# Kernel optimization log

Hardware: AMD Instinct MI355X
Metric: run time of the kernel (lower is better)

Reference implementation:

```python
import jax, jax.numpy as jnp
import numpy as np

DIM, HEADS, DIM_HEAD = 1024, 16, 64


def setup_inputs() -> dict:
    key = jax.random.key(0)
    k1, k2, k3, k4 = jax.random.split(key, 4)
    x = jax.random.normal(k1, (4, 2048, DIM), dtype=jnp.float32)
    # nn.Linear(dim, 3*dim, bias=False): weight [3*dim, dim]; y = x @ W.T
    W_qkv = jax.random.normal(k2, (3 * DIM, DIM), dtype=jnp.float32) * (DIM ** -0.5)
    W_proj = jax.random.normal(k3, (DIM, DIM), dtype=jnp.float32) * (DIM ** -0.5)
    b_proj = jax.random.normal(k4, (DIM,), dtype=jnp.float32) * 0.02
    return {"x": x, "W_qkv": W_qkv, "W_proj": W_proj, "b_proj": b_proj}


def reference(x, W_qkv, W_proj, b_proj):
    B, N, C = x.shape
    H, D = HEADS, DIM_HEAD
    scale = D ** -0.5
    qkv = x @ W_qkv.T                                   # [B, N, 3C]
    qkv = qkv.reshape(B, N, 3, H, D).transpose(2, 0, 3, 1, 4)  # [3, B, H, N, D]
    q, k, v = qkv[0], qkv[1], qkv[2]
    dots = jnp.einsum('bhid,bhjd->bhij', q, k) * scale  # [B, H, N, N]
    attn = jax.nn.softmax(dots, axis=-1)
    out = jnp.einsum('bhij,bhjd->bhid', attn, v)        # [B, H, N, D]
    out = out.transpose(0, 2, 1, 3).reshape(B, N, C)
    return out @ W_proj.T + b_proj
```

## Files before the change

kernel.cpp:

```cpp
#include <hip/hip_runtime.h>
#include <hip/hip_bf16.h>
#include <stdint.h>

typedef __bf16 bf16x4 __attribute__((ext_vector_type(4)));
typedef __bf16 bf16x8 __attribute__((ext_vector_type(8)));
typedef float  f32x4  __attribute__((ext_vector_type(4)));

#define LOG2E 1.44269504088896f

__device__ __forceinline__ void gl2lds16(const __bf16* g, __bf16* l) {
    __builtin_amdgcn_global_load_lds(
        (const __attribute__((address_space(1))) void*)g,
        (__attribute__((address_space(3))) void*)l, 16, 0, 0);
}

__global__ __launch_bounds__(256) void cvt_f32_bf16(const float* __restrict__ in,
                                                    __bf16* __restrict__ out) {
    size_t i = ((size_t)blockIdx.x * 256 + threadIdx.x) * 8;
    float4 a = ((const float4*)(in + i))[0];
    float4 b = ((const float4*)(in + i))[1];
    bf16x8 v;
    v[0] = (__bf16)a.x; v[1] = (__bf16)a.y; v[2] = (__bf16)a.z; v[3] = (__bf16)a.w;
    v[4] = (__bf16)b.x; v[5] = (__bf16)b.y; v[6] = (__bf16)b.z; v[7] = (__bf16)b.w;
    *(bf16x8*)(out + i) = v;
}

template<typename TC>
__global__ __launch_bounds__(256) void gemm_bt_bf16(
    const __bf16* __restrict__ A, const __bf16* __restrict__ B,
    const float* __restrict__ bias, TC* __restrict__ C,
    int M, int N, int K, int lda, int ldb, int ldc)
{
    __shared__ __bf16 As[128][32];
    __shared__ __bf16 Bs[128][32];
    const int tid = threadIdx.x;
    const int wave = tid >> 6, lane = tid & 63;
    const int lr = lane & 15, lq = lane >> 4;
    const int m0 = blockIdx.y * 128, n0 = blockIdx.x * 128;
    const int wm = (wave >> 1) * 64, wn = (wave & 1) * 64;

    f32x4 acc[4][4] = {};

    const int sr = lane >> 2;
    const int sc = (lane & 3) * 8;
    const __bf16* ag[2]; const __bf16* bg[2];
    __bf16* alds[2]; __bf16* blds[2];
    for (int t = 0; t < 2; ++t) {
        int chunk = wave * 2 + t;
        ag[t] = A + (size_t)(m0 + chunk * 16 + sr) * lda + sc;
        bg[t] = B + (size_t)(n0 + chunk * 16 + sr) * ldb + sc;
        alds[t] = &As[0][0] + chunk * 512;
        blds[t] = &Bs[0][0] + chunk * 512;
    }

    for (int k0 = 0; k0 < K; k0 += 32) {
        __syncthreads();
        gl2lds16(ag[0] + k0, alds[0]);
        gl2lds16(ag[1] + k0, alds[1]);
        gl2lds16(bg[0] + k0, blds[0]);
        gl2lds16(bg[1] + k0, blds[1]);
        __syncthreads();
        bf16x8 af[4], bf[4];
        for (int i = 0; i < 4; ++i) af[i] = *(const bf16x8*)&As[wm + i * 16 + lr][lq * 8];
        for (int j = 0; j < 4; ++j) bf[j] = *(const bf16x8*)&Bs[wn + j * 16 + lr][lq * 8];
        for (int i = 0; i < 4; ++i)
            for (int j = 0; j < 4; ++j)
                acc[i][j] = __builtin_amdgcn_mfma_f32_16x16x32_bf16(af[i], bf[j], acc[i][j], 0, 0, 0);
    }

    float bv[4] = {0.f, 0.f, 0.f, 0.f};
    if (bias)
        for (int j = 0; j < 4; ++j) bv[j] = bias[n0 + wn + j * 16 + lr];
    for (int i = 0; i < 4; ++i) {
        int row = m0 + wm + i * 16 + lq * 4;
        for (int j = 0; j < 4; ++j) {
            int col = n0 + wn + j * 16 + lr;
            for (int r = 0; r < 4; ++r) {
                float v = acc[i][j][r] + bv[j];
                C[(size_t)(row + r) * ldc + col] = (TC)v;
            }
        }
    }
}

__device__ __forceinline__ void stage16(const float* __restrict__ g, __bf16* l) {
    float4 a = ((const float4*)g)[0];
    float4 b = ((const float4*)g)[1];
    float4 c = ((const float4*)g)[2];
    float4 d = ((const float4*)g)[3];
    bf16x8 lo, hi;
    lo[0] = (__bf16)a.x; lo[1] = (__bf16)a.y; lo[2] = (__bf16)a.z; lo[3] = (__bf16)a.w;
    lo[4] = (__bf16)b.x; lo[5] = (__bf16)b.y; lo[6] = (__bf16)b.z; lo[7] = (__bf16)b.w;
    hi[0] = (__bf16)c.x; hi[1] = (__bf16)c.y; hi[2] = (__bf16)c.z; hi[3] = (__bf16)c.w;
    hi[4] = (__bf16)d.x; hi[5] = (__bf16)d.y; hi[6] = (__bf16)d.z; hi[7] = (__bf16)d.w;
    ((bf16x8*)l)[0] = lo;
    ((bf16x8*)l)[1] = hi;
}
__device__ __forceinline__ void stage16(const __bf16* __restrict__ g, __bf16* l) {
    ((bf16x8*)l)[0] = ((const bf16x8*)g)[0];
    ((bf16x8*)l)[1] = ((const bf16x8*)g)[1];
}

template<typename TA, typename TB, typename TC>
__global__ __launch_bounds__(256) void gemm_bt(
    const TA* __restrict__ A, const TB* __restrict__ B,
    const float* __restrict__ bias, TC* __restrict__ C,
    int M, int N, int K, int lda, int ldb, int ldc)
{
    __shared__ __bf16 As[128][40];
    __shared__ __bf16 Bs[128][40];
    const int tid = threadIdx.x;
    const int wave = tid >> 6, lane = tid & 63;
    const int lr = lane & 15, lq = lane >> 4;
    const int m0 = blockIdx.y * 128, n0 = blockIdx.x * 128;
    const int wm = (wave >> 1) * 64, wn = (wave & 1) * 64;
    const int srow = tid >> 1, scol = (tid & 1) * 16;

    f32x4 acc[4][4] = {};
    const TA* agp = A + (size_t)(m0 + srow) * lda + scol;
    const TB* bgp = B + (size_t)(n0 + srow) * ldb + scol;

    for (int k0 = 0; k0 < K; k0 += 32) {
        __syncthreads();
        stage16(agp + k0, &As[srow][scol]);
        stage16(bgp + k0, &Bs[srow][scol]);
        __syncthreads();
        bf16x8 af[4], bf[4];
        for (int i = 0; i < 4; ++i) af[i] = *(const bf16x8*)&As[wm + i * 16 + lr][lq * 8];
        for (int j = 0; j < 4; ++j) bf[j] = *(const bf16x8*)&Bs[wn + j * 16 + lr][lq * 8];
        for (int i = 0; i < 4; ++i)
            for (int j = 0; j < 4; ++j)
                acc[i][j] = __builtin_amdgcn_mfma_f32_16x16x32_bf16(af[i], bf[j], acc[i][j], 0, 0, 0);
    }

    float bv[4] = {0.f, 0.f, 0.f, 0.f};
    if (bias)
        for (int j = 0; j < 4; ++j) bv[j] = bias[n0 + wn + j * 16 + lr];
    for (int i = 0; i < 4; ++i) {
        int row = m0 + wm + i * 16 + lq * 4;
        for (int j = 0; j < 4; ++j) {
            int col = n0 + wn + j * 16 + lr;
            for (int r = 0; r < 4; ++r) {
                float v = acc[i][j][r] + bv[j];
                C[(size_t)(row + r) * ldc + col] = (TC)v;
            }
        }
    }
}

__global__ __launch_bounds__(256, 2) void attn_kernel(__bf16* __restrict__ qkv)
{
    __shared__ __bf16 Ks[2][64][72];
    __shared__ __bf16 Vt[2][64][72];

    const int tid = threadIdx.x;
    const int wave = tid >> 6, lane = tid & 63;
    const int lr = lane & 15, lq = lane >> 4;

    const int bid = blockIdx.x;
    const int xcd = bid & 7, slot = bid >> 3;
    const int bh = xcd * 8 + (slot >> 3);
    const int qt = slot & 7;
    const int b = bh >> 4, h = bh & 15;
    const int rowbase = b * 2048;
    const int q0 = qt * 256;
    const float c1 = 0.125f * LOG2E;

    bf16x8 qf[4][2];
    for (int mt = 0; mt < 4; ++mt)
        for (int ks = 0; ks < 2; ++ks) {
            bf16x8 v = *(const bf16x8*)(qkv +
                (size_t)(rowbase + q0 + wave * 64 + mt * 16 + lr) * 3072 + h * 64 + ks * 32 + lq * 8);
            bf16x8 w;
            for (int e = 0; e < 8; ++e) w[e] = (__bf16)((float)v[e] * c1);
            qf[mt][ks] = w;
        }

    bf16x8 ones8;
    for (int e = 0; e < 8; ++e) ones8[e] = (__bf16)1.0f;

    f32x4 l_acc[4] = {};
    f32x4 o_acc[4][4] = {};

    const int kr = tid >> 2, kc = (tid & 3) * 16;
    const int g0 = tid & 15;
    const int vj0 = g0 * 4, vd0 = (tid >> 4) * 4;
    const int vcol = ((g0 >> 3) * 32) + ((g0 & 3) * 8) + (((g0 >> 2) & 1) * 4);
    const __bf16* kbase = qkv + (size_t)(rowbase + kr) * 3072 + 1024 + h * 64 + kc;
    const __bf16* vbase = qkv + (size_t)(rowbase + vj0) * 3072 + 2048 + h * 64 + vd0;

    bf16x8 ka = ((const bf16x8*)kbase)[0];
    bf16x8 kb = ((const bf16x8*)kbase)[1];
    uint2 t0 = *(const uint2*)(vbase);
    uint2 t1 = *(const uint2*)(vbase + 3072);
    uint2 t2 = *(const uint2*)(vbase + 6144);
    uint2 t3 = *(const uint2*)(vbase + 9216);
    {
        *(bf16x8*)&Ks[0][kr][kc] = ka;
        *(bf16x8*)(&Ks[0][kr][kc] + 8) = kb;
        uint2 c0 = { (t0.x & 0xffffu) | (t1.x << 16), (t2.x & 0xffffu) | (t3.x << 16) };
        uint2 d1 = { (t0.x >> 16) | (t1.x & 0xffff0000u), (t2.x >> 16) | (t3.x & 0xffff0000u) };
        uint2 c2 = { (t0.y & 0xffffu) | (t1.y << 16), (t2.y & 0xffffu) | (t3.y << 16) };
        uint2 d3 = { (t0.y >> 16) | (t1.y & 0xffff0000u), (t2.y >> 16) | (t3.y & 0xffff0000u) };
        *(uint2*)&Vt[0][vd0 + 0][vcol] = c0;
        *(uint2*)&Vt[0][vd0 + 1][vcol] = d1;
        *(uint2*)&Vt[0][vd0 + 2][vcol] = c2;
        *(uint2*)&Vt[0][vd0 + 3][vcol] = d3;
    }

    for (int it = 0; it < 32; ++it) {
        const int cur = it & 1;
        __syncthreads();

        if (it + 1 < 32) {
            const __bf16* kg = kbase + (size_t)(it + 1) * 64 * 3072;
            ka = ((const bf16x8*)kg)[0];
            kb = ((const bf16x8*)kg)[1];
            const __bf16* vg = vbase + (size_t)(it + 1) * 64 * 3072;
            t0 = *(const uint2*)(vg);
            t1 = *(const uint2*)(vg + 3072);
            t2 = *(const uint2*)(vg + 6144);
            t3 = *(const uint2*)(vg + 9216);
        }

        for (int pi = 0; pi < 2; ++pi) {
            f32x4 s[4][2] = {};
            for (int ks = 0; ks < 2; ++ks) {
                bf16x8 kf0 = *(const bf16x8*)&Ks[cur][(2 * pi + 0) * 16 + lr][ks * 32 + lq * 8];
                bf16x8 kf1 = *(const bf16x8*)&Ks[cur][(2 * pi + 1) * 16 + lr][ks * 32 + lq * 8];
                for (int mt = 0; mt < 4; ++mt) {
                    s[mt][0] = __builtin_amdgcn_mfma_f32_16x16x32_bf16(kf0, qf[mt][ks], s[mt][0], 0, 0, 0);
                    s[mt][1] = __builtin_amdgcn_mfma_f32_16x16x32_bf16(kf1, qf[mt][ks], s[mt][1], 0, 0, 0);
                }
            }
            bf16x8 pfrag[4];
            for (int mt = 0; mt < 4; ++mt) {
                for (int t = 0; t < 2; ++t)
                    for (int r = 0; r < 4; ++r) {
                        float p = __builtin_amdgcn_exp2f(s[mt][t][r]);
                        pfrag[mt][t * 4 + r] = (__bf16)p;
                    }
            }
            for (int mt = 0; mt < 4; ++mt)
                l_acc[mt] = __builtin_amdgcn_mfma_f32_16x16x32_bf16(ones8, pfrag[mt], l_acc[mt], 0, 0, 0);
            for (int dt = 0; dt < 4; ++dt) {
                bf16x8 vf = *(const bf16x8*)&Vt[cur][dt * 16 + lr][pi * 32 + lq * 8];
                for (int mt = 0; mt < 4; ++mt)
                    o_acc[mt][dt] = __builtin_amdgcn_mfma_f32_16x16x32_bf16(vf, pfrag[mt], o_acc[mt][dt], 0, 0, 0);
            }
        }

        if (it + 1 < 32) {
            const int nb = cur ^ 1;
            *(bf16x8*)&Ks[nb][kr][kc] = ka;
            *(bf16x8*)(&Ks[nb][kr][kc] + 8) = kb;
            uint2 c0 = { (t0.x & 0xffffu) | (t1.x << 16), (t2.x & 0xffffu) | (t3.x << 16) };
            uint2 d1 = { (t0.x >> 16) | (t1.x & 0xffff0000u), (t2.x >> 16) | (t3.x & 0xffff0000u) };
            uint2 c2 = { (t0.y & 0xffffu) | (t1.y << 16), (t2.y & 0xffffu) | (t3.y << 16) };
            uint2 d3 = { (t0.y >> 16) | (t1.y & 0xffff0000u), (t2.y >> 16) | (t3.y & 0xffff0000u) };
            *(uint2*)&Vt[nb][vd0 + 0][vcol] = c0;
            *(uint2*)&Vt[nb][vd0 + 1][vcol] = d1;
            *(uint2*)&Vt[nb][vd0 + 2][vcol] = c2;
            *(uint2*)&Vt[nb][vd0 + 3][vcol] = d3;
        }
    }

    for (int mt = 0; mt < 4; ++mt) {
        float inv = 1.f / l_acc[mt][0];
        for (int dt = 0; dt < 4; ++dt) {
            bf16x4 ob;
            for (int r = 0; r < 4; ++r) ob[r] = (__bf16)(o_acc[mt][dt][r] * inv);
            *(bf16x4*)(qkv + (size_t)(rowbase + q0 + wave * 64 + mt * 16 + lr) * 3072 +
                       h * 64 + dt * 16 + lq * 4) = ob;
        }
    }
}

extern "C" void kernel_launch(void* const* d_in, const int* in_sizes, int n_in,
                              void* d_out, int out_size, void* d_ws, size_t ws_size,
                              hipStream_t stream) {
    const float* x     = (const float*)d_in[0];
    const float* Wqkv  = (const float*)d_in[1];
    const float* Wproj = (const float*)d_in[2];
    const float* bproj = (const float*)d_in[3];
    float* out   = (float*)d_out;
    __bf16* qkvb = (__bf16*)d_ws;

    const size_t QKV_E = (size_t)8192 * 3072;
    const size_t X_E   = (size_t)8192 * 1024;
    const size_t WQ_E  = (size_t)3072 * 1024;
    const size_t WP_E  = (size_t)1024 * 1024;
    const bool fast = ws_size >= (QKV_E + X_E + WQ_E + WP_E) * sizeof(__bf16);

    if (fast) {
        __bf16* xb  = qkvb + QKV_E;
        __bf16* wqb = xb + X_E;
        __bf16* wpb = wqb + WQ_E;
        cvt_f32_bf16<<<dim3((unsigned)(X_E / 2048)),  256, 0, stream>>>(x, xb);
        cvt_f32_bf16<<<dim3((unsigned)(WQ_E / 2048)), 256, 0, stream>>>(Wqkv, wqb);
        cvt_f32_bf16<<<dim3((unsigned)(WP_E / 2048)), 256, 0, stream>>>(Wproj, wpb);
        gemm_bt_bf16<__bf16><<<dim3(24, 64), 256, 0, stream>>>(
            xb, wqb, nullptr, qkvb, 8192, 3072, 1024, 1024, 1024, 3072);
        attn_kernel<<<dim3(512), 256, 0, stream>>>(qkvb);
        gemm_bt_bf16<float><<<dim3(8, 64), 256, 0, stream>>>(
            qkvb, wpb, bproj, out, 8192, 1024, 1024, 3072, 1024, 1024);
    } else {
        gemm_bt<float, float, __bf16><<<dim3(24, 64), 256, 0, stream>>>(
            x, Wqkv, nullptr, qkvb, 8192, 3072, 1024, 1024, 1024, 3072);
        attn_kernel<<<dim3(512), 256, 0, stream>>>(qkvb);
        gemm_bt<__bf16, float, float><<<dim3(8, 64), 256, 0, stream>>>(
            qkvb, Wproj, bproj, out, 8192, 1024, 1024, 3072, 1024, 1024);
    }
}
```

Before: 272.8 us.

## Split attention work across eight waves with K/V load specialization

The attention kernel now launches 512 threads per block instead of 256. Each wave handles 32 query rows instead of 64, which halves the per-wave accumulator registers. The K and V tile loads are split so waves 4-7 load K and waves 0-3 load and transpose V, instead of every thread loading both. The intent is more resident waves per CU to hide latency and a lighter per-thread load burden. The trade-off is that each wave now reads K/V fragments from LDS to reuse them over fewer query tiles, which lowers the MFMA-to-LDS-read ratio.

```diff
diff --git a/kernel.cpp b/kernel.cpp
--- a/kernel.cpp
+++ b/kernel.cpp
@@ -148,7 +148,7 @@
     }
 }
 
-__global__ __launch_bounds__(256, 2) void attn_kernel(__bf16* __restrict__ qkv)
+__global__ __launch_bounds__(512, 4) void attn_kernel(__bf16* __restrict__ qkv)
 {
     __shared__ __bf16 Ks[2][64][72];
     __shared__ __bf16 Vt[2][64][72];
@@ -166,11 +166,11 @@
     const int q0 = qt * 256;
     const float c1 = 0.125f * LOG2E;
 
-    bf16x8 qf[4][2];
-    for (int mt = 0; mt < 4; ++mt)
+    bf16x8 qf[2][2];
+    for (int mt = 0; mt < 2; ++mt)
         for (int ks = 0; ks < 2; ++ks) {
             bf16x8 v = *(const bf16x8*)(qkv +
-                (size_t)(rowbase + q0 + wave * 64 + mt * 16 + lr) * 3072 + h * 64 + ks * 32 + lq * 8);
+                (size_t)(rowbase + q0 + wave * 32 + mt * 16 + lr) * 3072 + h * 64 + ks * 32 + lq * 8);
             bf16x8 w;
             for (int e = 0; e < 8; ++e) w[e] = (__bf16)((float)v[e] * c1);
             qf[mt][ks] = w;
@@ -179,25 +179,30 @@
     bf16x8 ones8;
     for (int e = 0; e < 8; ++e) ones8[e] = (__bf16)1.0f;
 
-    f32x4 l_acc[4] = {};
-    f32x4 o_acc[4][4] = {};
-
-    const int kr = tid >> 2, kc = (tid & 3) * 16;
-    const int g0 = tid & 15;
-    const int vj0 = g0 * 4, vd0 = (tid >> 4) * 4;
+    f32x4 l_acc[2] = {};
+    f32x4 o_acc[2][4] = {};
+
+    const int tid2 = tid & 255;
+    const int kr = tid2 >> 2, kc = (tid2 & 3) * 16;
+    const int g0 = tid2 & 15;
+    const int vj0 = g0 * 4, vd0 = (tid2 >> 4) * 4;
     const int vcol = ((g0 >> 3) * 32) + ((g0 & 3) * 8) + (((g0 >> 2) & 1) * 4);
     const __bf16* kbase = qkv + (size_t)(rowbase + kr) * 3072 + 1024 + h * 64 + kc;
     const __bf16* vbase = qkv + (size_t)(rowbase + vj0) * 3072 + 2048 + h * 64 + vd0;
 
-    bf16x8 ka = ((const bf16x8*)kbase)[0];
-    bf16x8 kb = ((const bf16x8*)kbase)[1];
-    uint2 t0 = *(const uint2*)(vbase);
-    uint2 t1 = *(const uint2*)(vbase + 3072);
-    uint2 t2 = *(const uint2*)(vbase + 6144);
-    uint2 t3 = *(const uint2*)(vbase + 9216);
-    {
+    bf16x8 ka, kb;
+    uint2 t0, t1, t2, t3;
+
+    if (wave >= 4) {
+        ka = ((const bf16x8*)kbase)[0];
+        kb = ((const bf16x8*)kbase)[1];
         *(bf16x8*)&Ks[0][kr][kc] = ka;
         *(bf16x8*)(&Ks[0][kr][kc] + 8) = kb;
+    } else {
+        t0 = *(const uint2*)(vbase);
+        t1 = *(const uint2*)(vbase + 3072);
+        t2 = *(const uint2*)(vbase + 6144);
+        t3 = *(const uint2*)(vbase + 9216);
         uint2 c0 = { (t0.x & 0xffffu) | (t1.x << 16), (t2.x & 0xffffu) | (t3.x << 16) };
         uint2 d1 = { (t0.x >> 16) | (t1.x & 0xffff0000u), (t2.x >> 16) | (t3.x & 0xffff0000u) };
         uint2 c2 = { (t0.y & 0xffffu) | (t1.y << 16), (t2.y & 0xffffu) | (t3.y << 16) };
@@ -213,64 +218,70 @@
         __syncthreads();
 
         if (it + 1 < 32) {
-            const __bf16* kg = kbase + (size_t)(it + 1) * 64 * 3072;
-            ka = ((const bf16x8*)kg)[0];
-            kb = ((const bf16x8*)kg)[1];
-            const __bf16* vg = vbase + (size_t)(it + 1) * 64 * 3072;
-            t0 = *(const uint2*)(vg);
-            t1 = *(const uint2*)(vg + 3072);
-            t2 = *(const uint2*)(vg + 6144);
-            t3 = *(const uint2*)(vg + 9216);
+            if (wave >= 4) {
+                const __bf16* kg = kbase + (size_t)(it + 1) * 64 * 3072;
+                ka = ((const bf16x8*)kg)[0];
+                kb = ((const bf16x8*)kg)[1];
+            } else {
+                const __bf16* vg = vbase + (size_t)(it + 1) * 64 * 3072;
+                t0 = *(const uint2*)(vg);
+                t1 = *(const uint2*)(vg + 3072);
+                t2 = *(const uint2*)(vg + 6144);
+                t3 = *(const uint2*)(vg + 9216);
+            }
         }
 
         for (int pi = 0; pi < 2; ++pi) {
-            f32x4 s[4][2] = {};
+            f32x4 s[2][2] = {};
             for (int ks = 0; ks < 2; ++ks) {
                 bf16x8 kf0 = *(const bf16x8*)&Ks[cur][(2 * pi + 0) * 16 + lr][ks * 32 + lq * 8];
                 bf16x8 kf1 = *(const bf16x8*)&Ks[cur][(2 * pi + 1) * 16 + lr][ks * 32 + lq * 8];
-                for (int mt = 0; mt < 4; ++mt) {
+                for (int mt = 0; mt < 2; ++mt) {
                     s[mt][0] = __builtin_amdgcn_mfma_f32_16x16x32_bf16(kf0, qf[mt][ks], s[mt][0], 0, 0, 0);
                     s[mt][1] = __builtin_amdgcn_mfma_f32_16x16x32_bf16(kf1, qf[mt][ks], s[mt][1], 0, 0, 0);
                 }
             }
-            bf16x8 pfrag[4];
-            for (int mt = 0; mt < 4; ++mt) {
+            bf16x8 pfrag[2];
+            for (int mt = 0; mt < 2; ++mt) {
                 for (int t = 0; t < 2; ++t)
                     for (int r = 0; r < 4; ++r) {
                         float p = __builtin_amdgcn_exp2f(s[mt][t][r]);
                         pfrag[mt][t * 4 + r] = (__bf16)p;
                     }
             }
-            for (int mt = 0; mt < 4; ++mt)
+            for (int mt = 0; mt < 2; ++mt)
                 l_acc[mt] = __builtin_amdgcn_mfma_f32_16x16x32_bf16(ones8, pfrag[mt], l_acc[mt], 0, 0, 0);
             for (int dt = 0; dt < 4; ++dt) {
                 bf16x8 vf = *(const bf16x8*)&Vt[cur][dt * 16 + lr][pi * 32 + lq * 8];
-                for (int mt = 0; mt < 4; ++mt)
+                for (int mt = 0; mt < 2; ++mt)
                     o_acc[mt][dt] = __builtin_amdgcn_mfma_f32_16x16x32_bf16(vf, pfrag[mt], o_acc[mt][dt], 0, 0, 0);
             }
         }
 
         if (it + 1 < 32) {
             const int nb = cur ^ 1;
-            *(bf16x8*)&Ks[nb][kr][kc] = ka;
-            *(bf16x8*)(&Ks[nb][kr][kc] + 8) = kb;
-            uint2 c0 = { (t0.x & 0xffffu) | (t1.x << 16), (t2.x & 0xffffu) | (t3.x << 16) };
-            uint2 d1 = { (t0.x >> 16) | (t1.x & 0xffff0000u), (t2.x >> 16) | (t3.x & 0xffff0000u) };
-            uint2 c2 = { (t0.y & 0xffffu) | (t1.y << 16), (t2.y & 0xffffu) | (t3.y << 16) };
-            uint2 d3 = { (t0.y >> 16) | (t1.y & 0xffff0000u), (t2.y >> 16) | (t3.y & 0xffff0000u) };
-            *(uint2*)&Vt[nb][vd0 + 0][vcol] = c0;
-            *(uint2*)&Vt[nb][vd0 + 1][vcol] = d1;
-            *(uint2*)&Vt[nb][vd0 + 2][vcol] = c2;
-            *(uint2*)&Vt[nb][vd0 + 3][vcol] = d3;
-        }
-    }
-
-    for (int mt = 0; mt < 4; ++mt) {
+            if (wave >= 4) {
+                *(bf16x8*)&Ks[nb][kr][kc] = ka;
+                *(bf16x8*)(&Ks[nb][kr][kc] + 8) = kb;
+            } else {
+                uint2 c0 = { (t0.x & 0xffffu) | (t1.x << 16), (t2.x & 0xffffu) | (t3.x << 16) };
+                uint2 d1 = { (t0.x >> 16) | (t1.x & 0xffff0000u), (t2.x >> 16) | (t3.x & 0xffff0000u) };
+                uint2 c2 = { (t0.y & 0xffffu) | (t1.y << 16), (t2.y & 0xffffu) | (t3.y << 16) };
+                uint2 d3 = { (t0.y >> 16) | (t1.y & 0xffff0000u), (t2.y >> 16) | (t3.y & 0xffff0000u) };
+                *(uint2*)&Vt[nb][vd0 + 0][vcol] = c0;
+                *(uint2*)&Vt[nb][vd0 + 1][vcol] = d1;
+                *(uint2*)&Vt[nb][vd0 + 2][vcol] = c2;
+                *(uint2*)&Vt[nb][vd0 + 3][vcol] = d3;
+            }
+        }
+    }
+
+    for (int mt = 0; mt < 2; ++mt) {
         float inv = 1.f / l_acc[mt][0];
         for (int dt = 0; dt < 4; ++dt) {
             bf16x4 ob;
             for (int r = 0; r < 4; ++r) ob[r] = (__bf16)(o_acc[mt][dt][r] * inv);
-            *(bf16x4*)(qkv + (size_t)(rowbase + q0 + wave * 64 + mt * 16 + lr) * 3072 +
+            *(bf16x4*)(qkv + (size_t)(rowbase + q0 + wave * 32 + mt * 16 + lr) * 3072 +
                        h * 64 + dt * 16 + lq * 4) = ob;
         }
     }
@@ -301,13 +312,13 @@
         cvt_f32_bf16<<<dim3((unsigned)(WP_E / 2048)), 256, 0, stream>>>(Wproj, wpb);
         gemm_bt_bf16<__bf16><<<dim3(24, 64), 256, 0, stream>>>(
             xb, wqb, nullptr, qkvb, 8192, 3072, 1024, 1024, 1024, 3072);
-        attn_kernel<<<dim3(512), 256, 0, stream>>>(qkvb);
+        attn_kernel<<<dim3(512), 512, 0, stream>>>(qkvb);
         gemm_bt_bf16<float><<<dim3(8, 64), 256, 0, stream>>>(
             qkvb, wpb, bproj, out, 8192, 1024, 1024, 3072, 1024, 1024);
     } else {
         gemm_bt<float, float, __bf16><<<dim3(24, 64), 256, 0, stream>>>(
             x, Wqkv, nullptr, qkvb, 8192, 3072, 1024, 1024, 1024, 3072);
-        attn_kernel<<<dim3(512), 256, 0, stream>>>(qkvb);
+        attn_kernel<<<dim3(512), 512, 0, stream>>>(qkvb);
         gemm_bt<__bf16, float, float><<<dim3(8, 64), 256, 0, stream>>>(
             qkvb, Wproj, bproj, out, 8192, 1024, 1024, 3072, 1024, 1024);
     }
```

Result: faster. 266.5 us (-2.3%).
